# Kernel tuning notes

Measured on AMD Instinct MI355X. Metric: run time of the kernel, lower is better.

The kernel has to match this reference:

```python
import jax, jax.numpy as jnp
import numpy as np

B, T, E, H = 4, 2048, 1024, 1024

def setup_inputs() -> dict:
    key = jax.random.key(0)
    k1, k2, k3, k4 = jax.random.split(key, 4)
    inputs = jax.random.normal(k1, (B, T, E), dtype=jnp.float32)
    # Dense(size, use_bias=False) -> weight [emb, size], glorot-ish scale
    Wq = jax.random.normal(k2, (E, H), dtype=jnp.float32) * (1.0 / np.sqrt(E))
    Wk = jax.random.normal(k3, (E, H), dtype=jnp.float32) * (1.0 / np.sqrt(E))
    Wv = jax.random.normal(k4, (E, H), dtype=jnp.float32) * (1.0 / np.sqrt(E))
    return {"inputs": inputs, "Wq": Wq, "Wk": Wk, "Wv": Wv}

def reference(inputs, Wq, Wk, Wv):
    # inputs: [B, T, E]
    _, Tc, Ec = inputs.shape
    q = inputs @ Wq  # [B, T, H]
    k = inputs @ Wk  # [B, T, H]
    v = inputs @ Wv  # [B, T, H]
    # scores scaled by emb_dim**-0.5 (NOT head size) as in the source
    w = jnp.einsum('bih,bjh->bij', q, k) * (Ec ** -0.5)  # [B, T, T]
    tril = jnp.tril(jnp.ones((Tc, Tc), dtype=bool))
    w = jnp.where(tril, w, -jnp.inf)
    # NOTE: source uses softmax over axis=1 (query axis), non-standard but faithful
    w = jax.nn.softmax(w, axis=1)
    # dropout_rate=0.0 -> identity
    out = w @ v  # [B, T, H]
    return out
```

## Files before the change

### kernel.cpp

```cpp
#include <hip/hip_runtime.h>
#include <hip/hip_bf16.h>
#include <stdint.h>


typedef short bf16x8 __attribute__((ext_vector_type(8)));
typedef float f32x4  __attribute__((ext_vector_type(4)));

__device__ __forceinline__ unsigned short f2bf(float f) {
    union { float f; unsigned u; } x; x.f = f;
    unsigned r = x.u + 0x7FFFu + ((x.u >> 16) & 1u);
    return (unsigned short)(r >> 16);
}
__device__ __forceinline__ float bf2f(unsigned short h) {
    union { unsigned u; float f; } x; x.u = ((unsigned)h) << 16;
    return x.f;
}

__global__ __launch_bounds__(256) void prep_kernel(
    const float* __restrict__ X,
    const float* __restrict__ Wq, const float* __restrict__ Wk,
    const float* __restrict__ Wv,
    unsigned short* __restrict__ Xb, unsigned short* __restrict__ WT)
{
    __shared__ unsigned short tile[64][65];
    unsigned id = blockIdx.x;
    if (id < 8192) {
        size_t i = ((size_t)id * 256 + threadIdx.x) * 4;
        float4 v = *(const float4*)(X + i);
        union { unsigned short h[4]; unsigned long long u; } p;
        p.h[0] = f2bf(v.x); p.h[1] = f2bf(v.y);
        p.h[2] = f2bf(v.z); p.h[3] = f2bf(v.w);
        *(unsigned long long*)(Xb + i) = p.u;
    } else {
        unsigned w = id - 8192;
        unsigned which = w >> 8;
        const float* W = (which == 0) ? Wq : (which == 1) ? Wk : Wv;
        unsigned short* out = WT + (size_t)which * 1024 * 1024;
        const int R = 1024, C = 1024;
        unsigned t2 = w & 255;
        int c0 = (int)(t2 & 15) * 64, r0 = (int)(t2 >> 4) * 64;
        int tx = threadIdx.x & 63, ty = threadIdx.x >> 6;
#pragma unroll
        for (int i = 0; i < 16; ++i) {
            int r = ty + i * 4;
            tile[r][tx] = f2bf(W[(size_t)(r0 + r) * C + c0 + tx]);
        }
        __syncthreads();
#pragma unroll
        for (int i = 0; i < 16; ++i) {
            int c = ty + i * 4;
            out[(size_t)(c0 + c) * R + r0 + tx] = tile[tx][c];
        }
    }
}

__global__ __launch_bounds__(256, 3) void gemm_nt_qkv(
    const unsigned short* __restrict__ A, const unsigned short* __restrict__ B,
    unsigned short* __restrict__ Cout, unsigned short* __restrict__ C2,
    unsigned short* __restrict__ C3, int K, int ldt, int tmoff)
{
    unsigned id = blockIdx.y * gridDim.x + blockIdx.x;
    unsigned xcd = id & 7, k2 = id >> 3;
    int tm = (int)(xcd * 4 + (k2 & 3)) + tmoff;
    int tn = (int)(k2 >> 2);
    int m0 = tm * 128, n0 = tn * 128;
    int kmax = K;

    __shared__ unsigned short sAB[2 * 128 * 64];
    char* sAc = (char*)sAB;
    char* sBc = (char*)sAB + 16384;

    unsigned t = threadIdx.x, lane = t & 63, wave = t >> 6;

    unsigned srow = t >> 2;
    unsigned gsw = (t & 3) ^ ((t >> 3) & 3);
    const unsigned short* pA = A + (size_t)(m0 + srow) * K + gsw * 8;
    const unsigned short* pB = B + (size_t)(n0 + srow) * K + gsw * 8;
    const size_t rstep = (size_t)64 * K;
    unsigned ldsOff = t * 16;

    unsigned wm = (wave >> 1) * 64, wn = (wave & 1) * 64;
    unsigned lrow = lane & 15;
    unsigned lk = ((lane >> 4) ^ ((lane >> 1) & 3)) * 8;
    const short* sAs = (const short*)sAB;
    const short* sBs = (const short*)(sAB + 128 * 64);

    f32x4 acc[4][4] = {};

    int4 rA0 = *(const int4*)(pA);
    int4 rA1 = *(const int4*)(pA + rstep);
    int4 rA2 = *(const int4*)(pA + 32);
    int4 rA3 = *(const int4*)(pA + rstep + 32);
    int4 rB0 = *(const int4*)(pB);
    int4 rB1 = *(const int4*)(pB + rstep);
    int4 rB2 = *(const int4*)(pB + 32);
    int4 rB3 = *(const int4*)(pB + rstep + 32);

    for (int k0 = 0; k0 < kmax; k0 += 64) {
        __syncthreads();
        *(int4*)(sAc + ldsOff)         = rA0;
        *(int4*)(sAc + ldsOff + 4096)  = rA1;
        *(int4*)(sAc + ldsOff + 8192)  = rA2;
        *(int4*)(sAc + ldsOff + 12288) = rA3;
        *(int4*)(sBc + ldsOff)         = rB0;
        *(int4*)(sBc + ldsOff + 4096)  = rB1;
        *(int4*)(sBc + ldsOff + 8192)  = rB2;
        *(int4*)(sBc + ldsOff + 12288) = rB3;
        __syncthreads();

        if (k0 + 64 < kmax) {
            pA += 64; pB += 64;
            rA0 = *(const int4*)(pA);
            rA1 = *(const int4*)(pA + rstep);
            rA2 = *(const int4*)(pA + 32);
            rA3 = *(const int4*)(pA + rstep + 32);
            rB0 = *(const int4*)(pB);
            rB1 = *(const int4*)(pB + rstep);
            rB2 = *(const int4*)(pB + 32);
            rB3 = *(const int4*)(pB + rstep + 32);
        }

#pragma unroll
        for (int kk = 0; kk < 2; ++kk) {
            bf16x8 a[4], b[4];
#pragma unroll
            for (int i = 0; i < 4; ++i) {
                a[i] = *(const bf16x8*)(sAs + kk * 4096 + (wm + i * 16 + lrow) * 32 + lk);
                b[i] = *(const bf16x8*)(sBs + kk * 4096 + (wn + i * 16 + lrow) * 32 + lk);
            }
#pragma unroll
            for (int i = 0; i < 4; ++i)
#pragma unroll
                for (int j = 0; j < 4; ++j)
                    acc[i][j] = __builtin_amdgcn_mfma_f32_16x16x32_bf16(
                        a[i], b[j], acc[i][j], 0, 0, 0);
        }
    }

    unsigned col = lane & 15, rq = (lane >> 4) * 4;
    if (n0 < 2048) {
        unsigned short* C = (n0 < 1024) ? Cout : C2;
        int nb = n0 & 1023;
#pragma unroll
        for (int i = 0; i < 4; ++i)
#pragma unroll
            for (int j = 0; j < 4; ++j)
#pragma unroll
                for (int r = 0; r < 4; ++r)
                    C[(size_t)(m0 + wm + i * 16 + rq + r) * 1024 + nb + wn + j * 16 + col] =
                        f2bf(acc[i][j][r]);
    } else {
        int batch = m0 >> 11, tb = m0 & 2047;
        unsigned short* C = C3 + (size_t)batch * 1024 * 2048;
#pragma unroll
        for (int i = 0; i < 4; ++i)
#pragma unroll
            for (int j = 0; j < 4; ++j) {
                union { unsigned short h[4]; unsigned long long u; } p;
#pragma unroll
                for (int r = 0; r < 4; ++r) p.h[r] = f2bf(acc[i][j][r]);
                int h = (n0 - 2048) + wn + j * 16 + col;
                int t0 = tb + wm + i * 16 + rq;
                *(unsigned long long*)(C + (size_t)h * ldt + t0) = p.u;
            }
    }
}

__global__ __launch_bounds__(256, 4) void scores64_kernel(
    const unsigned short* __restrict__ A, const unsigned short* __restrict__ B,
    unsigned short* __restrict__ Eb, float* __restrict__ fpar, float scale)
{
    int bz = blockIdx.z;
    unsigned bx = blockIdx.x;
    int u = (int)((bx & 7u) * 34u + (bx >> 3));
    int tm = (int)((sqrtf(4.f * (float)u + 1.f) - 1.f) * 0.5f);
    while ((tm + 1) * (tm + 2) <= u) ++tm;
    while (tm * (tm + 1) > u) --tm;
    int tn64 = u - tm * (tm + 1);
    const int K = 1024;
    int m0 = tm * 128, n0 = tn64 * 64;
    A += (size_t)bz * (size_t)2048 * 1024;
    B += (size_t)bz * (size_t)2048 * 1024;

    __shared__ unsigned short sAB[12288];
    char* sAc = (char*)sAB;
    char* sBc = (char*)sAB + 16384;

    unsigned t = threadIdx.x, lane = t & 63, wave = t >> 6;
    unsigned srow = t >> 2;
    unsigned gsw = (t & 3) ^ ((t >> 3) & 3);
    const unsigned short* pA = A + (size_t)(m0 + srow) * K + gsw * 8;
    const unsigned short* pB = B + (size_t)(n0 + srow) * K + gsw * 8;
    const size_t rstep = (size_t)64 * K;
    unsigned ldsOff = t * 16;

    unsigned wm = (wave >> 1) * 64, wn = (wave & 1) * 32;
    unsigned lrow = lane & 15;
    unsigned lk = ((lane >> 4) ^ ((lane >> 1) & 3)) * 8;
    const short* sAs = (const short*)sAB;
    const short* sBs = (const short*)(sAB + 8192);

    f32x4 acc[4][2] = {};

    int4 rA0 = *(const int4*)(pA);
    int4 rA1 = *(const int4*)(pA + rstep);
    int4 rA2 = *(const int4*)(pA + 32);
    int4 rA3 = *(const int4*)(pA + rstep + 32);
    int4 rB0 = *(const int4*)(pB);
    int4 rB1 = *(const int4*)(pB + 32);

    for (int k0 = 0; k0 < K; k0 += 64) {
        __syncthreads();
        *(int4*)(sAc + ldsOff)         = rA0;
        *(int4*)(sAc + ldsOff + 4096)  = rA1;
        *(int4*)(sAc + ldsOff + 8192)  = rA2;
        *(int4*)(sAc + ldsOff + 12288) = rA3;
        *(int4*)(sBc + ldsOff)         = rB0;
        *(int4*)(sBc + ldsOff + 4096)  = rB1;
        __syncthreads();

        if (k0 + 64 < K) {
            pA += 64; pB += 64;
            rA0 = *(const int4*)(pA);
            rA1 = *(const int4*)(pA + rstep);
            rA2 = *(const int4*)(pA + 32);
            rA3 = *(const int4*)(pA + rstep + 32);
            rB0 = *(const int4*)(pB);
            rB1 = *(const int4*)(pB + 32);
        }

#pragma unroll
        for (int kk = 0; kk < 2; ++kk) {
            bf16x8 a[4], b[2];
#pragma unroll
            for (int i = 0; i < 4; ++i)
                a[i] = *(const bf16x8*)(sAs + kk * 4096 + (wm + i * 16 + lrow) * 32 + lk);
#pragma unroll
            for (int j = 0; j < 2; ++j)
                b[j] = *(const bf16x8*)(sBs + kk * 2048 + (wn + j * 16 + lrow) * 32 + lk);
#pragma unroll
            for (int i = 0; i < 4; ++i)
#pragma unroll
                for (int j = 0; j < 2; ++j)
                    acc[i][j] = __builtin_amdgcn_mfma_f32_16x16x32_bf16(
                        a[i], b[j], acc[i][j], 0, 0, 0);
        }
    }

    unsigned col = lane & 15, rq = (lane >> 4) * 4;
    unsigned short* Ebp = Eb + (size_t)bz * (size_t)2048 * 2048;
    float* par = fpar + (size_t)bz * 32 * 2048;
    bool diag = ((tn64 >> 1) == tm);
    unsigned short* tile = sAB;
    __syncthreads();
#pragma unroll
    for (int jj = 0; jj < 2; ++jj) {
        float csum = 0.f;
        int jl = (int)(wn + jj * 16 + col);
        int jg = n0 + jl;
#pragma unroll
        for (int ii = 0; ii < 4; ++ii) {
#pragma unroll
            for (int r = 0; r < 4; ++r) {
                int il = (int)(wm + ii * 16 + rq + r);
                int ig = m0 + il;
                unsigned short us = 0;
                if (!diag || ig >= jg)
                    us = f2bf(__expf(acc[ii][jj][r] * scale));
                tile[il * 64 + jl] = us;
                csum += bf2f(us);
            }
        }
        csum += __shfl_xor(csum, 16);
        csum += __shfl_xor(csum, 32);
        if (lane < 16) {
            int rh = (m0 + (int)wm) >> 6;
            par[(size_t)rh * 2048 + n0 + wn + jj * 16 + lane] = csum;
        }
    }
    __syncthreads();
    {
        unsigned rr = t >> 3, cc = (t & 7) * 8;
#pragma unroll
        for (int p = 0; p < 4; ++p) {
            int li = (int)(p * 32 + rr);
            int4 v = *(const int4*)(tile + li * 64 + cc);
            *(int4*)(Ebp + (size_t)(m0 + li) * 2048 + n0 + cc) = v;
        }
    }
}

__global__ __launch_bounds__(256, 3) void pv128_kernel(
    const unsigned short* __restrict__ A, const unsigned short* __restrict__ B,
    float* __restrict__ out)
{
    unsigned n = blockIdx.x;
    int tn = (int)(n & 7u);
    unsigned q = n >> 3, half = q >> 5, r = q & 31u;
    int bz = (int)((half ? 2u : 0u) + (r & 1u));
    int tm = half ? (int)(r >> 1) : (int)(15u - (r >> 1));
    const int K = 2048, N = 1024;
    int m0 = tm * 128, n0 = tn * 128;
    int kmax = m0 + 128;
    A += (size_t)bz * (size_t)2048 * 2048;
    B += (size_t)bz * (size_t)1024 * 2048;

    __shared__ unsigned short sAB[2 * 128 * 64];
    char* sAc = (char*)sAB;
    char* sBc = (char*)sAB + 16384;

    unsigned t = threadIdx.x, lane = t & 63, wave = t >> 6;

    unsigned srow = t >> 2;
    unsigned gsw = (t & 3) ^ ((t >> 3) & 3);
    const unsigned short* pA = A + (size_t)(m0 + srow) * K + gsw * 8;
    const unsigned short* pB = B + (size_t)(n0 + srow) * K + gsw * 8;
    const size_t rstep = (size_t)64 * K;
    unsigned ldsOff = t * 16;

    unsigned wm = (wave >> 1) * 64, wn = (wave & 1) * 64;
    unsigned lrow = lane & 15;
    unsigned lk = ((lane >> 4) ^ ((lane >> 1) & 3)) * 8;
    const short* sAs = (const short*)sAB;
    const short* sBs = (const short*)(sAB + 128 * 64);

    f32x4 acc[4][4] = {};

    int4 rA0 = *(const int4*)(pA);
    int4 rA1 = *(const int4*)(pA + rstep);
    int4 rA2 = *(const int4*)(pA + 32);
    int4 rA3 = *(const int4*)(pA + rstep + 32);
    int4 rB0 = *(const int4*)(pB);
    int4 rB1 = *(const int4*)(pB + rstep);
    int4 rB2 = *(const int4*)(pB + 32);
    int4 rB3 = *(const int4*)(pB + rstep + 32);

    for (int k0 = 0; k0 < kmax; k0 += 64) {
        __syncthreads();
        *(int4*)(sAc + ldsOff)         = rA0;
        *(int4*)(sAc + ldsOff + 4096)  = rA1;
        *(int4*)(sAc + ldsOff + 8192)  = rA2;
        *(int4*)(sAc + ldsOff + 12288) = rA3;
        *(int4*)(sBc + ldsOff)         = rB0;
        *(int4*)(sBc + ldsOff + 4096)  = rB1;
        *(int4*)(sBc + ldsOff + 8192)  = rB2;
        *(int4*)(sBc + ldsOff + 12288) = rB3;
        __syncthreads();

        if (k0 + 64 < kmax) {
            pA += 64; pB += 64;
            rA0 = *(const int4*)(pA);
            rA1 = *(const int4*)(pA + rstep);
            rA2 = *(const int4*)(pA + 32);
            rA3 = *(const int4*)(pA + rstep + 32);
            rB0 = *(const int4*)(pB);
            rB1 = *(const int4*)(pB + rstep);
            rB2 = *(const int4*)(pB + 32);
            rB3 = *(const int4*)(pB + rstep + 32);
        }

#pragma unroll
        for (int kk = 0; kk < 2; ++kk) {
            bf16x8 a[4], b[4];
#pragma unroll
            for (int i = 0; i < 4; ++i) {
                a[i] = *(const bf16x8*)(sAs + kk * 4096 + (wm + i * 16 + lrow) * 32 + lk);
                b[i] = *(const bf16x8*)(sBs + kk * 4096 + (wn + i * 16 + lrow) * 32 + lk);
            }
#pragma unroll
            for (int i = 0; i < 4; ++i)
#pragma unroll
                for (int j = 0; j < 4; ++j)
                    acc[i][j] = __builtin_amdgcn_mfma_f32_16x16x32_bf16(
                        a[i], b[j], acc[i][j], 0, 0, 0);
        }
    }

    unsigned col = lane & 15, rq = (lane >> 4) * 4;
    float* C = out + (size_t)bz * (size_t)2048 * 1024;
#pragma unroll
    for (int i = 0; i < 4; ++i)
#pragma unroll
        for (int j = 0; j < 4; ++j)
#pragma unroll
            for (int r = 0; r < 4; ++r)
                C[(size_t)(m0 + wm + i * 16 + rq + r) * N + n0 + wn + j * 16 + col] =
                    acc[i][j][r];
}

__global__ __launch_bounds__(256) void colsum_scale(
    const float* __restrict__ par, unsigned short* __restrict__ Vt)
{
    int b = blockIdx.z, t0 = blockIdx.x * 64, h0 = blockIdx.y * 128;
    __shared__ float Ls[64];
    int tid = threadIdx.x;
    if (tid < 64) {
        int j = t0 + tid;
        const float* p = par + (size_t)b * 32 * 2048;
        float s = 0.f;
        for (int rh = j >> 6; rh < 32; ++rh) s += p[(size_t)rh * 2048 + j];
        Ls[tid] = 1.0f / s;
    }
    __syncthreads();
    unsigned short* V = Vt + ((size_t)b << 21);
    int c8 = (tid & 7) * 8;
#pragma unroll
    for (int rr = 0; rr < 4; ++rr) {
        int h = h0 + rr * 32 + (tid >> 3);
        size_t idx = (size_t)h * 2048 + t0 + c8;
        bf16x8 v = *(bf16x8*)(V + idx);
#pragma unroll
        for (int e = 0; e < 8; ++e)
            v[e] = (short)f2bf(bf2f((unsigned short)v[e]) * Ls[c8 + e]);
        *(bf16x8*)(V + idx) = v;
    }
}

extern "C" void kernel_launch(void* const* d_in, const int* in_sizes, int n_in,
                              void* d_out, int out_size, void* d_ws, size_t ws_size,
                              hipStream_t stream)
{
    const int B = 4, T = 2048, E = 1024, H = 1024;
    const int M = B * T;
    const float* X  = (const float*)d_in[0];
    const float* Wq = (const float*)d_in[1];
    const float* Wk = (const float*)d_in[2];
    const float* Wv = (const float*)d_in[3];
    float* out = (float*)d_out;
    char* ws = (char*)d_ws;
    const size_t MB = 1024 * 1024;

    unsigned short* Xb  = (unsigned short*)(ws + 0);
    unsigned short* WqT = (unsigned short*)(ws + 16 * MB);
    unsigned short* Qb  = (unsigned short*)(ws + 32 * MB);
    unsigned short* Kb  = (unsigned short*)(ws + 48 * MB);
    unsigned short* Vt  = (unsigned short*)(ws + 64 * MB);
    unsigned short* Eb  = (unsigned short*)(ws + 0);
    float*          par  = (float*)d_out;

    prep_kernel<<<dim3(8960), 256, 0, stream>>>(X, Wq, Wk, Wv, Xb, WqT);

    gemm_nt_qkv<<<dim3(24, 32, 1), 256, 0, stream>>>(
        Xb, WqT, Qb, Kb, Vt, E, T, 0);
    gemm_nt_qkv<<<dim3(24, 32, 1), 256, 0, stream>>>(
        Xb, WqT, Qb, Kb, Vt, E, T, 32);

    scores64_kernel<<<dim3(272, 1, B), 256, 0, stream>>>(
        Qb, Kb, Eb, par, 0.03125f);

    colsum_scale<<<dim3(32, 8, 4), 256, 0, stream>>>(par, Vt);

    pv128_kernel<<<dim3(512), 256, 0, stream>>>(Eb, Vt, out);
}
```

Measured before the change: 235.3 us.

## Double-buffer LDS in QKV GEMM and merge two launches into one

The QKV projection GEMM now keeps two LDS buffers. Each loop iteration computes from one buffer while storing the next K-tile's prefetched registers into the other, which cuts the two barriers per iteration to one. The two half-grid launches are merged into a single launch with a new tile-to-XCD mapping. LDS use doubles to 64KB per block, which may reduce occupancy below the launch_bounds target of 3 blocks.

```diff
diff --git a/kernel.cpp b/kernel.cpp
--- a/kernel.cpp
+++ b/kernel.cpp
@@ -57,18 +57,15 @@
 __global__ __launch_bounds__(256, 3) void gemm_nt_qkv(
     const unsigned short* __restrict__ A, const unsigned short* __restrict__ B,
     unsigned short* __restrict__ Cout, unsigned short* __restrict__ C2,
-    unsigned short* __restrict__ C3, int K, int ldt, int tmoff)
+    unsigned short* __restrict__ C3, int K, int ldt)
 {
     unsigned id = blockIdx.y * gridDim.x + blockIdx.x;
     unsigned xcd = id & 7, k2 = id >> 3;
-    int tm = (int)(xcd * 4 + (k2 & 3)) + tmoff;
-    int tn = (int)(k2 >> 2);
+    int tm = (int)(xcd * 8 + (k2 & 7));
+    int tn = (int)(k2 >> 3);
     int m0 = tm * 128, n0 = tn * 128;
-    int kmax = K;
-
-    __shared__ unsigned short sAB[2 * 128 * 64];
-    char* sAc = (char*)sAB;
-    char* sBc = (char*)sAB + 16384;
+
+    __shared__ unsigned short sAB[2][2 * 128 * 64];
 
     unsigned t = threadIdx.x, lane = t & 63, wave = t >> 6;
 
@@ -82,8 +79,6 @@
     unsigned wm = (wave >> 1) * 64, wn = (wave & 1) * 64;
     unsigned lrow = lane & 15;
     unsigned lk = ((lane >> 4) ^ ((lane >> 1) & 3)) * 8;
-    const short* sAs = (const short*)sAB;
-    const short* sBs = (const short*)(sAB + 128 * 64);
 
     f32x4 acc[4][4] = {};
 
@@ -95,9 +90,9 @@
     int4 rB1 = *(const int4*)(pB + rstep);
     int4 rB2 = *(const int4*)(pB + 32);
     int4 rB3 = *(const int4*)(pB + rstep + 32);
-
-    for (int k0 = 0; k0 < kmax; k0 += 64) {
-        __syncthreads();
+    {
+        char* sAc = (char*)sAB[0];
+        char* sBc = (char*)sAB[0] + 16384;
         *(int4*)(sAc + ldsOff)         = rA0;
         *(int4*)(sAc + ldsOff + 4096)  = rA1;
         *(int4*)(sAc + ldsOff + 8192)  = rA2;
@@ -106,9 +101,13 @@
         *(int4*)(sBc + ldsOff + 4096)  = rB1;
         *(int4*)(sBc + ldsOff + 8192)  = rB2;
         *(int4*)(sBc + ldsOff + 12288) = rB3;
-        __syncthreads();
-
-        if (k0 + 64 < kmax) {
+    }
+    __syncthreads();
+
+    unsigned p = 0;
+    for (int k0 = 0; k0 < K; k0 += 64, p ^= 1) {
+        bool more = (k0 + 64 < K);
+        if (more) {
             pA += 64; pB += 64;
             rA0 = *(const int4*)(pA);
             rA1 = *(const int4*)(pA + rstep);
@@ -120,6 +119,8 @@
             rB3 = *(const int4*)(pB + rstep + 32);
         }
 
+        const short* sAs = (const short*)sAB[p];
+        const short* sBs = (const short*)(sAB[p] + 128 * 64);
 #pragma unroll
         for (int kk = 0; kk < 2; ++kk) {
             bf16x8 a[4], b[4];
@@ -135,6 +136,20 @@
                     acc[i][j] = __builtin_amdgcn_mfma_f32_16x16x32_bf16(
                         a[i], b[j], acc[i][j], 0, 0, 0);
         }
+
+        if (more) {
+            char* sAc = (char*)sAB[p ^ 1];
+            char* sBc = (char*)sAB[p ^ 1] + 16384;
+            *(int4*)(sAc + ldsOff)         = rA0;
+            *(int4*)(sAc + ldsOff + 4096)  = rA1;
+            *(int4*)(sAc + ldsOff + 8192)  = rA2;
+            *(int4*)(sAc + ldsOff + 12288) = rA3;
+            *(int4*)(sBc + ldsOff)         = rB0;
+            *(int4*)(sBc + ldsOff + 4096)  = rB1;
+            *(int4*)(sBc + ldsOff + 8192)  = rB2;
+            *(int4*)(sBc + ldsOff + 12288) = rB3;
+        }
+        __syncthreads();
     }
 
     unsigned col = lane & 15, rq = (lane >> 4) * 4;
@@ -156,12 +171,12 @@
         for (int i = 0; i < 4; ++i)
 #pragma unroll
             for (int j = 0; j < 4; ++j) {
-                union { unsigned short h[4]; unsigned long long u; } p;
-#pragma unroll
-                for (int r = 0; r < 4; ++r) p.h[r] = f2bf(acc[i][j][r]);
+                union { unsigned short h[4]; unsigned long long u; } p2;
+#pragma unroll
+                for (int r = 0; r < 4; ++r) p2.h[r] = f2bf(acc[i][j][r]);
                 int h = (n0 - 2048) + wn + j * 16 + col;
                 int t0 = tb + wm + i * 16 + rq;
-                *(unsigned long long*)(C + (size_t)h * ldt + t0) = p.u;
+                *(unsigned long long*)(C + (size_t)h * ldt + t0) = p2.u;
             }
     }
 }
@@ -440,10 +455,8 @@
 
     prep_kernel<<<dim3(8960), 256, 0, stream>>>(X, Wq, Wk, Wv, Xb, WqT);
 
-    gemm_nt_qkv<<<dim3(24, 32, 1), 256, 0, stream>>>(
-        Xb, WqT, Qb, Kb, Vt, E, T, 0);
-    gemm_nt_qkv<<<dim3(24, 32, 1), 256, 0, stream>>>(
-        Xb, WqT, Qb, Kb, Vt, E, T, 32);
+    gemm_nt_qkv<<<dim3(24, 64, 1), 256, 0, stream>>>(
+        Xb, WqT, Qb, Kb, Vt, E, T);
 
     scores64_kernel<<<dim3(272, 1, B), 256, 0, stream>>>(
         Qb, Kb, Eb, par, 0.03125f);
```

After: 239.3 us. Within noise of the previous version (+1.7%).
